# Kernel tuning notes

Measured on AMD Instinct MI355X. Metric: run time of the kernel, lower is better.

## Reference

```python
import jax, jax.numpy as jnp
import numpy as np
import math

# kinematic tree: parent of each of the 23 joints (parents[i] < i -> topological order)
PARENTS = np.array([-1, 0, 1, 1, 3, 4, 5, 4, 7, 4, 9, 1, 11, 12, 13, 12, 15, 12, 17, 0, 19, 0, 21])
NUM_J = 23
HALF, QUART = math.pi / 2.0, math.pi / 4.0
# (joint slot, scale) for the pose params actually written in the torch forward
POSE_SLOTS = [(0, QUART), (3, HALF), (4, HALF), (5, QUART), (7, QUART), (9, QUART),
              (11, HALF), (12, HALF), (13, QUART), (15, QUART), (17, QUART)]


def _rodrigues(r):
    # r: [..., 3] axis-angle -> [..., 3, 3] rotation matrix
    angle = jnp.sqrt(jnp.sum(r * r, axis=-1) + 1e-16)
    axis = r / angle[..., None]
    s, c = jnp.sin(angle), jnp.cos(angle)
    x, y, z = axis[..., 0], axis[..., 1], axis[..., 2]
    zero = jnp.zeros_like(x)
    K = jnp.stack([jnp.stack([zero, -z, y], -1),
                   jnp.stack([z, zero, -x], -1),
                   jnp.stack([-y, x, zero], -1)], -2)
    I = jnp.eye(3, dtype=r.dtype)
    return I + s[..., None, None] * K + (1.0 - c)[..., None, None] * (K @ K)


def _lbs_forward(vertices, joints, weights, displacement, random_dis, pose_params):
    P = displacement.shape[0]
    dt = vertices.dtype
    # per-joint pose: pi/4 or pi/2 * tanh(param) on the used slots, zeros elsewhere
    pose = jnp.zeros((P, NUM_J, 3), dt)
    for (idx, scale), prm in zip(POSE_SLOTS, pose_params):
        pose = pose.at[:, idx].set(scale * jnp.tanh(prm))
    R = _rodrigues(pose)                                          # [P,J,3,3]
    j = joints[0].astype(dt)                                      # [J,3] rest joints
    rel = jnp.concatenate([j[:1], j[1:] - j[PARENTS[1:]]], 0)     # joint offsets from parent
    top = jnp.concatenate([R, jnp.broadcast_to(rel[None, :, :, None], (P, NUM_J, 3, 1))], -1)
    bot = jnp.broadcast_to(jnp.array([0.0, 0.0, 0.0, 1.0], dt), (P, NUM_J, 1, 4))
    T_local = jnp.concatenate([top, bot], -2)                     # [P,J,4,4]
    # forward-kinematics tree walk (fixed 23-joint chain, parents precede children)
    Gs = [T_local[:, 0]]
    for i in range(1, NUM_J):
        Gs.append(Gs[PARENTS[i]] @ T_local[:, i])
    G = jnp.stack(Gs, 1)                                          # [P,J,4,4]
    posed_joints = G[..., :3, 3]                                  # [P,J,3]
    # A = G - [0 | G_rot @ j_rest]  (keep only the 3x4 part actually needed)
    A = G[:, :, :3, :].at[..., 3].add(-jnp.einsum('pjab,jb->pja', G[:, :, :3, :3], j))  # [P,J,3,4]
    W = weights.astype(dt)
    T = jnp.einsum('vj,pjab->pvab', W, A)                         # [P,V,3,4] skinning transforms
    v = vertices[0]                                               # [V,3]
    v_posed = jnp.einsum('pvij,vj->pvi', T[..., :3], v) + T[..., 3]  # [P,V,3]
    shift = random_dis[:, None, :] + 3.0 * jnp.tanh(displacement)   # [P,1,3]
    return v_posed + shift, posed_joints + shift


def setup_inputs():
    P, V, J = 16, 500000, NUM_J
    key = jax.random.key(0)
    ks = jax.random.split(key, 16)
    w = jax.random.uniform(ks[2], (V, J), jnp.float32)
    inp = {
        'vertices': jax.random.normal(ks[0], (1, V, 3), jnp.float32),
        'joints': jax.random.normal(ks[1], (1, J, 3), jnp.float32),
        'weights': w / jnp.sum(w, -1, keepdims=True),  # convex skinning weights
        'displacement': 0.1 * jax.random.normal(ks[3], (P, 1, 3), jnp.float32),
        'random_dis': jax.random.normal(ks[4], (P, 3), jnp.float32),
    }
    names = ['joint_0', 'joint_3', 'joint_4', 'joint_5', 'joint_7', 'joint_9',
             'joint_11', 'joint_12', 'joint_13', 'joint_15', 'joint_17']
    for i, n in enumerate(names):
        inp[n] = jax.random.normal(ks[5 + i], (P, 3), jnp.float32)
    return inp


def reference(vertices, joints, weights, displacement, random_dis, joint_0, joint_3, joint_4, joint_5, joint_7, joint_9, joint_11, joint_12, joint_13, joint_15, joint_17):
    pose_params = (joint_0, joint_3, joint_4, joint_5, joint_7, joint_9,
                   joint_11, joint_12, joint_13, joint_15, joint_17)
    return _lbs_forward(vertices, joints, weights, displacement, random_dis, pose_params)
```

## Files before the change

### kernel.cpp

```cpp
#include <hip/hip_runtime.h>
#include <hip/hip_bf16.h>

typedef __hip_bfloat16 bf16;

#define P_CNT 16
#define J_CNT 23

__device__ int    g_flag;
__device__ float4 g_A[P_CNT * J_CNT * 3];
__device__ float  g_shift[P_CNT * 3];

struct PosePtrs { const void* p[11]; };

template <bool BF>
__device__ __forceinline__ float ld(const void* p, long long i) {
    if (BF) return __bfloat162float(((const bf16*)p)[i]);
    return ((const float*)p)[i];
}
template <bool BF>
__device__ __forceinline__ void st(void* p, long long i, float v) {
    if (BF) ((bf16*)p)[i] = __float2bfloat16(v);
    else    ((float*)p)[i] = v;
}

__global__ void detect_kernel(const void* __restrict__ w) {
    if (threadIdx.x != 0 || blockIdx.x != 0) return;
    const float* wf = (const float*)w;
    const bf16*  wb = (const bf16*)w;
    bool ok_f = true, ok_b = true;
    for (int r = 0; r < 4; ++r) {
        float sf = 0.f, sb = 0.f;
        for (int j = 0; j < J_CNT; ++j) {
            sf += wf[r * J_CNT + j];
            sb += __bfloat162float(wb[r * J_CNT + j]);
        }
        if (!(fabsf(sf - 1.f) < 0.02f)) ok_f = false;
        if (!(fabsf(sb - 1.f) < 0.10f)) ok_b = false;
    }
    g_flag = (!ok_f && ok_b) ? 1 : 0;
}

template <bool BF>
__global__ void pose_kernel(const void* __restrict__ joints,
                            const void* __restrict__ disp,
                            const void* __restrict__ rdis,
                            PosePtrs pp,
                            void* __restrict__ out1)
{
    if (g_flag != (BF ? 1 : 0)) return;
    __shared__ float Gs[P_CNT][J_CNT][12];
    int p = threadIdx.x;
    if (p >= P_CNT) return;

    const int par[J_CNT]     = {-1,0,1,1,3,4,5,4,7,4,9,1,11,12,13,12,15,12,17,0,19,0,21};
    const int slot_of[J_CNT] = {0,-1,-1,1,2,3,-1,4,-1,5,-1,6,7,8,-1,9,-1,10,-1,-1,-1,-1,-1};
    const float slot_sc[11]  = {
        0.7853981633974483f, 1.5707963267948966f, 1.5707963267948966f, 0.7853981633974483f,
        0.7853981633974483f, 0.7853981633974483f, 1.5707963267948966f, 1.5707963267948966f,
        0.7853981633974483f, 0.7853981633974483f, 0.7853981633974483f};

    for (int j = 0; j < J_CNT; ++j) {
        float rx = 0.f, ry = 0.f, rz = 0.f;
        int s = slot_of[j];
        if (s >= 0) {
            float sc = slot_sc[s];
            rx = sc * tanhf(ld<BF>(pp.p[s], p * 3 + 0));
            ry = sc * tanhf(ld<BF>(pp.p[s], p * 3 + 1));
            rz = sc * tanhf(ld<BF>(pp.p[s], p * 3 + 2));
        }
        float ang = sqrtf(rx * rx + ry * ry + rz * rz + 1e-16f);
        float sn = sinf(ang), cs = cosf(ang);
        float C = 1.f - cs;
        float inva = 1.f / ang;
        float x = rx * inva, y = ry * inva, z = rz * inva;
        float R[3][3];
        R[0][0] = 1.f - C * (y * y + z * z); R[0][1] = -sn * z + C * x * y;       R[0][2] = sn * y + C * x * z;
        R[1][0] = sn * z + C * x * y;        R[1][1] = 1.f - C * (x * x + z * z); R[1][2] = -sn * x + C * y * z;
        R[2][0] = -sn * y + C * x * z;       R[2][1] = sn * x + C * y * z;        R[2][2] = 1.f - C * (x * x + y * y);

        int q = par[j];
        float t[3];
        for (int c = 0; c < 3; ++c) {
            float jc = ld<BF>(joints, j * 3 + c);
            t[c] = (j == 0) ? jc : (jc - ld<BF>(joints, q * 3 + c));
        }
        if (j == 0) {
            for (int i = 0; i < 3; ++i) {
                Gs[p][0][i * 4 + 0] = R[i][0];
                Gs[p][0][i * 4 + 1] = R[i][1];
                Gs[p][0][i * 4 + 2] = R[i][2];
                Gs[p][0][i * 4 + 3] = t[i];
            }
        } else {
            for (int i = 0; i < 3; ++i) {
                float g0 = Gs[p][q][i * 4 + 0], g1 = Gs[p][q][i * 4 + 1];
                float g2 = Gs[p][q][i * 4 + 2], g3 = Gs[p][q][i * 4 + 3];
                Gs[p][j][i * 4 + 0] = g0 * R[0][0] + g1 * R[1][0] + g2 * R[2][0];
                Gs[p][j][i * 4 + 1] = g0 * R[0][1] + g1 * R[1][1] + g2 * R[2][1];
                Gs[p][j][i * 4 + 2] = g0 * R[0][2] + g1 * R[1][2] + g2 * R[2][2];
                Gs[p][j][i * 4 + 3] = g0 * t[0] + g1 * t[1] + g2 * t[2] + g3;
            }
        }
    }

    float sh[3];
    for (int c = 0; c < 3; ++c) {
        sh[c] = ld<BF>(rdis, p * 3 + c) + 3.f * tanhf(ld<BF>(disp, p * 3 + c));
        g_shift[p * 3 + c] = sh[c];
    }

    for (int j = 0; j < J_CNT; ++j) {
        float jx = ld<BF>(joints, j * 3 + 0);
        float jy = ld<BF>(joints, j * 3 + 1);
        float jz = ld<BF>(joints, j * 3 + 2);
        for (int i = 0; i < 3; ++i) {
            float g0 = Gs[p][j][i * 4 + 0], g1 = Gs[p][j][i * 4 + 1];
            float g2 = Gs[p][j][i * 4 + 2], g3 = Gs[p][j][i * 4 + 3];
            g_A[(p * J_CNT + j) * 3 + i] =
                make_float4(g0, g1, g2, g3 - (g0 * jx + g1 * jy + g2 * jz));
            st<BF>(out1, (p * J_CNT + j) * 3 + i, g3 + sh[i]);
        }
    }
}

template <bool BF>
__global__ __launch_bounds__(256) void lbs_vertex(
    const void* __restrict__ verts,
    const void* __restrict__ weights,
    void* __restrict__ out0,
    int V)
{
    if (g_flag != (BF ? 1 : 0)) return;
    __shared__ float4 As[P_CNT * J_CNT * 3];
    __shared__ float  sh[P_CNT * 3];
    for (int i = threadIdx.x; i < P_CNT * J_CNT * 3; i += 256) As[i] = g_A[i];
    for (int i = threadIdx.x; i < P_CNT * 3; i += 256) sh[i] = g_shift[i];
    __syncthreads();

    int v = blockIdx.x * 256 + threadIdx.x;
    if (v >= V) return;

    float w[J_CNT];
    long long wbase = (long long)v * J_CNT;
#pragma unroll
    for (int j = 0; j < J_CNT; ++j) w[j] = ld<BF>(weights, wbase + j);
    float x = ld<BF>(verts, (long long)v * 3 + 0);
    float y = ld<BF>(verts, (long long)v * 3 + 1);
    float z = ld<BF>(verts, (long long)v * 3 + 2);

    for (int p = 0; p < P_CNT; ++p) {
        const float4* Ap = As + p * (J_CNT * 3);
        float4 t0 = make_float4(0.f, 0.f, 0.f, 0.f);
        float4 t1 = make_float4(0.f, 0.f, 0.f, 0.f);
        float4 t2 = make_float4(0.f, 0.f, 0.f, 0.f);
#pragma unroll
        for (int j = 0; j < J_CNT; ++j) {
            float wj = w[j];
            float4 a0 = Ap[j * 3 + 0], a1 = Ap[j * 3 + 1], a2 = Ap[j * 3 + 2];
            t0.x = fmaf(wj, a0.x, t0.x); t0.y = fmaf(wj, a0.y, t0.y);
            t0.z = fmaf(wj, a0.z, t0.z); t0.w = fmaf(wj, a0.w, t0.w);
            t1.x = fmaf(wj, a1.x, t1.x); t1.y = fmaf(wj, a1.y, t1.y);
            t1.z = fmaf(wj, a1.z, t1.z); t1.w = fmaf(wj, a1.w, t1.w);
            t2.x = fmaf(wj, a2.x, t2.x); t2.y = fmaf(wj, a2.y, t2.y);
            t2.z = fmaf(wj, a2.z, t2.z); t2.w = fmaf(wj, a2.w, t2.w);
        }
        float ox = fmaf(t0.x, x, fmaf(t0.y, y, fmaf(t0.z, z, t0.w))) + sh[p * 3 + 0];
        float oy = fmaf(t1.x, x, fmaf(t1.y, y, fmaf(t1.z, z, t1.w))) + sh[p * 3 + 1];
        float oz = fmaf(t2.x, x, fmaf(t2.y, y, fmaf(t2.z, z, t2.w))) + sh[p * 3 + 2];
        long long base = ((long long)p * V + v) * 3;
        st<BF>(out0, base + 0, ox);
        st<BF>(out0, base + 1, oy);
        st<BF>(out0, base + 2, oz);
    }
}

extern "C" void kernel_launch(void* const* d_in, const int* in_sizes, int n_in,
                              void* d_out, int out_size, void* d_ws, size_t ws_size,
                              hipStream_t stream) {
    const void* verts   = d_in[0];
    const void* joints  = d_in[1];
    const void* weights = d_in[2];
    const void* disp    = d_in[3];
    const void* rdis    = d_in[4];
    PosePtrs pp;
    for (int i = 0; i < 11; ++i) pp.p[i] = d_in[5 + i];

    int V = in_sizes[0] / 3;
    long long pv3 = (long long)P_CNT * V * 3;

    void* out1_f = (void*)((float*)d_out + pv3);
    void* out1_b = (void*)((bf16*) d_out + pv3);

    detect_kernel<<<1, 64, 0, stream>>>(weights);
    pose_kernel<false><<<1, 64, 0, stream>>>(joints, disp, rdis, pp, out1_f);
    pose_kernel<true ><<<1, 64, 0, stream>>>(joints, disp, rdis, pp, out1_b);
    int G = (V + 255) / 256;
    lbs_vertex<false><<<G, 256, 0, stream>>>(verts, weights, d_out, V);
    lbs_vertex<true ><<<G, 256, 0, stream>>>(verts, weights, d_out, V);
}
```

Baseline: 252.8 us.

## Drop runtime dtype detection and process four vertices per thread

Removes the bf16/fp32 detection kernel and the duplicate template launches, so only the fp32 pose and vertex kernels run. The vertex kernel now handles four vertices per thread, so each shared-memory load of a joint transform feeds four vertices' FMAs and LDS traffic per FMA falls. Register use grows (4x23 weights plus 48 accumulators), which may cut occupancy or cause spills. The pose loop is no longer unrolled, and fp32 inputs are now assumed.

After: 559.8 us. 121% more time.

```diff
diff --git a/kernel.cpp b/kernel.cpp
--- a/kernel.cpp
+++ b/kernel.cpp
@@ -1,53 +1,21 @@
 #include <hip/hip_runtime.h>
 #include <hip/hip_bf16.h>
 
-typedef __hip_bfloat16 bf16;
-
 #define P_CNT 16
 #define J_CNT 23
+#define VPT   4
 
-__device__ int    g_flag;
 __device__ float4 g_A[P_CNT * J_CNT * 3];
 __device__ float  g_shift[P_CNT * 3];
 
-struct PosePtrs { const void* p[11]; };
+struct PosePtrs { const float* p[11]; };
 
-template <bool BF>
-__device__ __forceinline__ float ld(const void* p, long long i) {
-    if (BF) return __bfloat162float(((const bf16*)p)[i]);
-    return ((const float*)p)[i];
-}
-template <bool BF>
-__device__ __forceinline__ void st(void* p, long long i, float v) {
-    if (BF) ((bf16*)p)[i] = __float2bfloat16(v);
-    else    ((float*)p)[i] = v;
-}
-
-__global__ void detect_kernel(const void* __restrict__ w) {
-    if (threadIdx.x != 0 || blockIdx.x != 0) return;
-    const float* wf = (const float*)w;
-    const bf16*  wb = (const bf16*)w;
-    bool ok_f = true, ok_b = true;
-    for (int r = 0; r < 4; ++r) {
-        float sf = 0.f, sb = 0.f;
-        for (int j = 0; j < J_CNT; ++j) {
-            sf += wf[r * J_CNT + j];
-            sb += __bfloat162float(wb[r * J_CNT + j]);
-        }
-        if (!(fabsf(sf - 1.f) < 0.02f)) ok_f = false;
-        if (!(fabsf(sb - 1.f) < 0.10f)) ok_b = false;
-    }
-    g_flag = (!ok_f && ok_b) ? 1 : 0;
-}
-
-template <bool BF>
-__global__ void pose_kernel(const void* __restrict__ joints,
-                            const void* __restrict__ disp,
-                            const void* __restrict__ rdis,
+__global__ void pose_kernel(const float* __restrict__ joints,
+                            const float* __restrict__ disp,
+                            const float* __restrict__ rdis,
                             PosePtrs pp,
-                            void* __restrict__ out1)
+                            float* __restrict__ out1)
 {
-    if (g_flag != (BF ? 1 : 0)) return;
     __shared__ float Gs[P_CNT][J_CNT][12];
     int p = threadIdx.x;
     if (p >= P_CNT) return;
@@ -64,9 +32,9 @@
         int s = slot_of[j];
         if (s >= 0) {
             float sc = slot_sc[s];
-            rx = sc * tanhf(ld<BF>(pp.p[s], p * 3 + 0));
-            ry = sc * tanhf(ld<BF>(pp.p[s], p * 3 + 1));
-            rz = sc * tanhf(ld<BF>(pp.p[s], p * 3 + 2));
+            rx = sc * tanhf(pp.p[s][p * 3 + 0]);
+            ry = sc * tanhf(pp.p[s][p * 3 + 1]);
+            rz = sc * tanhf(pp.p[s][p * 3 + 2]);
         }
         float ang = sqrtf(rx * rx + ry * ry + rz * rz + 1e-16f);
         float sn = sinf(ang), cs = cosf(ang);
@@ -81,8 +49,8 @@
         int q = par[j];
         float t[3];
         for (int c = 0; c < 3; ++c) {
-            float jc = ld<BF>(joints, j * 3 + c);
-            t[c] = (j == 0) ? jc : (jc - ld<BF>(joints, q * 3 + c));
+            float jc = joints[j * 3 + c];
+            t[c] = (j == 0) ? jc : (jc - joints[q * 3 + c]);
         }
         if (j == 0) {
             for (int i = 0; i < 3; ++i) {
@@ -105,96 +73,112 @@
 
     float sh[3];
     for (int c = 0; c < 3; ++c) {
-        sh[c] = ld<BF>(rdis, p * 3 + c) + 3.f * tanhf(ld<BF>(disp, p * 3 + c));
+        sh[c] = rdis[p * 3 + c] + 3.f * tanhf(disp[p * 3 + c]);
         g_shift[p * 3 + c] = sh[c];
     }
 
     for (int j = 0; j < J_CNT; ++j) {
-        float jx = ld<BF>(joints, j * 3 + 0);
-        float jy = ld<BF>(joints, j * 3 + 1);
-        float jz = ld<BF>(joints, j * 3 + 2);
+        float jx = joints[j * 3 + 0];
+        float jy = joints[j * 3 + 1];
+        float jz = joints[j * 3 + 2];
         for (int i = 0; i < 3; ++i) {
             float g0 = Gs[p][j][i * 4 + 0], g1 = Gs[p][j][i * 4 + 1];
             float g2 = Gs[p][j][i * 4 + 2], g3 = Gs[p][j][i * 4 + 3];
             g_A[(p * J_CNT + j) * 3 + i] =
                 make_float4(g0, g1, g2, g3 - (g0 * jx + g1 * jy + g2 * jz));
-            st<BF>(out1, (p * J_CNT + j) * 3 + i, g3 + sh[i]);
+            out1[(p * J_CNT + j) * 3 + i] = g3 + sh[i];
         }
     }
 }
 
-template <bool BF>
 __global__ __launch_bounds__(256) void lbs_vertex(
-    const void* __restrict__ verts,
-    const void* __restrict__ weights,
-    void* __restrict__ out0,
+    const float* __restrict__ verts,
+    const float* __restrict__ weights,
+    float* __restrict__ out0,
     int V)
 {
-    if (g_flag != (BF ? 1 : 0)) return;
     __shared__ float4 As[P_CNT * J_CNT * 3];
     __shared__ float  sh[P_CNT * 3];
     for (int i = threadIdx.x; i < P_CNT * J_CNT * 3; i += 256) As[i] = g_A[i];
     for (int i = threadIdx.x; i < P_CNT * 3; i += 256) sh[i] = g_shift[i];
     __syncthreads();
 
-    int v = blockIdx.x * 256 + threadIdx.x;
-    if (v >= V) return;
+    const int lane = threadIdx.x & 63;
+    const int wv   = threadIdx.x >> 6;
+    const long long vbase = (long long)blockIdx.x * (256 * VPT) + wv * (64 * VPT) + lane;
 
-    float w[J_CNT];
-    long long wbase = (long long)v * J_CNT;
+    long long vi[VPT];
+    bool ok[VPT];
+    float w[VPT][J_CNT];
+    float X[VPT], Y[VPT], Z[VPT];
 #pragma unroll
-    for (int j = 0; j < J_CNT; ++j) w[j] = ld<BF>(weights, wbase + j);
-    float x = ld<BF>(verts, (long long)v * 3 + 0);
-    float y = ld<BF>(verts, (long long)v * 3 + 1);
-    float z = ld<BF>(verts, (long long)v * 3 + 2);
+    for (int k = 0; k < VPT; ++k) {
+        long long v = vbase + k * 64;
+        ok[k] = (v < V);
+        vi[k] = ok[k] ? v : (V - 1);
+        const float* wr = weights + vi[k] * J_CNT;
+#pragma unroll
+        for (int j = 0; j < J_CNT; ++j) w[k][j] = wr[j];
+        X[k] = verts[vi[k] * 3 + 0];
+        Y[k] = verts[vi[k] * 3 + 1];
+        Z[k] = verts[vi[k] * 3 + 2];
+    }
 
+#pragma unroll 1
     for (int p = 0; p < P_CNT; ++p) {
+        float4 t0[VPT], t1[VPT], t2[VPT];
+#pragma unroll
+        for (int k = 0; k < VPT; ++k) {
+            t0[k] = make_float4(0.f, 0.f, 0.f, 0.f);
+            t1[k] = make_float4(0.f, 0.f, 0.f, 0.f);
+            t2[k] = make_float4(0.f, 0.f, 0.f, 0.f);
+        }
         const float4* Ap = As + p * (J_CNT * 3);
-        float4 t0 = make_float4(0.f, 0.f, 0.f, 0.f);
-        float4 t1 = make_float4(0.f, 0.f, 0.f, 0.f);
-        float4 t2 = make_float4(0.f, 0.f, 0.f, 0.f);
 #pragma unroll
         for (int j = 0; j < J_CNT; ++j) {
-            float wj = w[j];
             float4 a0 = Ap[j * 3 + 0], a1 = Ap[j * 3 + 1], a2 = Ap[j * 3 + 2];
-            t0.x = fmaf(wj, a0.x, t0.x); t0.y = fmaf(wj, a0.y, t0.y);
-            t0.z = fmaf(wj, a0.z, t0.z); t0.w = fmaf(wj, a0.w, t0.w);
-            t1.x = fmaf(wj, a1.x, t1.x); t1.y = fmaf(wj, a1.y, t1.y);
-            t1.z = fmaf(wj, a1.z, t1.z); t1.w = fmaf(wj, a1.w, t1.w);
-            t2.x = fmaf(wj, a2.x, t2.x); t2.y = fmaf(wj, a2.y, t2.y);
-            t2.z = fmaf(wj, a2.z, t2.z); t2.w = fmaf(wj, a2.w, t2.w);
+#pragma unroll
+            for (int k = 0; k < VPT; ++k) {
+                float wj = w[k][j];
+                t0[k].x = fmaf(wj, a0.x, t0[k].x); t0[k].y = fmaf(wj, a0.y, t0[k].y);
+                t0[k].z = fmaf(wj, a0.z, t0[k].z); t0[k].w = fmaf(wj, a0.w, t0[k].w);
+                t1[k].x = fmaf(wj, a1.x, t1[k].x); t1[k].y = fmaf(wj, a1.y, t1[k].y);
+                t1[k].z = fmaf(wj, a1.z, t1[k].z); t1[k].w = fmaf(wj, a1.w, t1[k].w);
+                t2[k].x = fmaf(wj, a2.x, t2[k].x); t2[k].y = fmaf(wj, a2.y, t2[k].y);
+                t2[k].z = fmaf(wj, a2.z, t2[k].z); t2[k].w = fmaf(wj, a2.w, t2[k].w);
+            }
         }
-        float ox = fmaf(t0.x, x, fmaf(t0.y, y, fmaf(t0.z, z, t0.w))) + sh[p * 3 + 0];
-        float oy = fmaf(t1.x, x, fmaf(t1.y, y, fmaf(t1.z, z, t1.w))) + sh[p * 3 + 1];
-        float oz = fmaf(t2.x, x, fmaf(t2.y, y, fmaf(t2.z, z, t2.w))) + sh[p * 3 + 2];
-        long long base = ((long long)p * V + v) * 3;
-        st<BF>(out0, base + 0, ox);
-        st<BF>(out0, base + 1, oy);
-        st<BF>(out0, base + 2, oz);
+        float shx = sh[p * 3 + 0], shy = sh[p * 3 + 1], shz = sh[p * 3 + 2];
+#pragma unroll
+        for (int k = 0; k < VPT; ++k) {
+            if (!ok[k]) continue;
+            float ox = fmaf(t0[k].x, X[k], fmaf(t0[k].y, Y[k], fmaf(t0[k].z, Z[k], t0[k].w))) + shx;
+            float oy = fmaf(t1[k].x, X[k], fmaf(t1[k].y, Y[k], fmaf(t1[k].z, Z[k], t1[k].w))) + shy;
+            float oz = fmaf(t2[k].x, X[k], fmaf(t2[k].y, Y[k], fmaf(t2[k].z, Z[k], t2[k].w))) + shz;
+            long long base = ((long long)p * V + vi[k]) * 3;
+            out0[base + 0] = ox;
+            out0[base + 1] = oy;
+            out0[base + 2] = oz;
+        }
     }
 }
 
 extern "C" void kernel_launch(void* const* d_in, const int* in_sizes, int n_in,
                               void* d_out, int out_size, void* d_ws, size_t ws_size,
                               hipStream_t stream) {
-    const void* verts   = d_in[0];
-    const void* joints  = d_in[1];
-    const void* weights = d_in[2];
-    const void* disp    = d_in[3];
-    const void* rdis    = d_in[4];
+    const float* verts   = (const float*)d_in[0];
+    const float* joints  = (const float*)d_in[1];
+    const float* weights = (const float*)d_in[2];
+    const float* disp    = (const float*)d_in[3];
+    const float* rdis    = (const float*)d_in[4];
     PosePtrs pp;
-    for (int i = 0; i < 11; ++i) pp.p[i] = d_in[5 + i];
+    for (int i = 0; i < 11; ++i) pp.p[i] = (const float*)d_in[5 + i];
 
     int V = in_sizes[0] / 3;
-    long long pv3 = (long long)P_CNT * V * 3;
+    float* out0 = (float*)d_out;
+    float* out1 = out0 + (long long)P_CNT * V * 3;
 
-    void* out1_f = (void*)((float*)d_out + pv3);
-    void* out1_b = (void*)((bf16*) d_out + pv3);
-
-    detect_kernel<<<1, 64, 0, stream>>>(weights);
-    pose_kernel<false><<<1, 64, 0, stream>>>(joints, disp, rdis, pp, out1_f);
-    pose_kernel<true ><<<1, 64, 0, stream>>>(joints, disp, rdis, pp, out1_b);
-    int G = (V + 255) / 256;
-    lbs_vertex<false><<<G, 256, 0, stream>>>(verts, weights, d_out, V);
-    lbs_vertex<true ><<<G, 256, 0, stream>>>(verts, weights, d_out, V);
+    pose_kernel<<<1, 64, 0, stream>>>(joints, disp, rdis, pp, out1);
+    int G = (V + 256 * VPT - 1) / (256 * VPT);
+    lbs_vertex<<<G, 256, 0, stream>>>(verts, weights, out0, V);
 }
```
